# Optimization experiments

Hardware: AMD Instinct MI355X
Metric: run time of the kernel (lower is better)

The kernel has to match this reference:

```python
import jax, jax.numpy as jnp
import numpy as np

N_NODES = 20000
N_EDGES = 160000
N_GRAPHS = 64
IN_DIM = 128
HID = 512
N_ACT = 32


def gcn_conv(x, W, b, src, dst, n_nodes):
    # PyG GCNConv: add self-loops, symmetric normalization, x @ W then scatter-add.
    loop = jnp.arange(n_nodes, dtype=src.dtype)
    s = jnp.concatenate([src, loop])
    d = jnp.concatenate([dst, loop])
    deg = jax.ops.segment_sum(jnp.ones_like(d, dtype=x.dtype), d, num_segments=n_nodes)
    dinv = jnp.where(deg > 0, jax.lax.rsqrt(deg), 0.0)
    norm = dinv[s] * dinv[d]                      # [E+N]
    h = x @ W                                     # [N, out]
    msg = h[s] * norm[:, None]                    # gather + scale
    out = jax.ops.segment_sum(msg, d, num_segments=n_nodes)
    return out + b


def setup_inputs() -> dict:
    key = jax.random.key(0)
    ks = jax.random.split(key, 16)
    tree_x = jax.random.normal(ks[0], (N_NODES, IN_DIM), dtype=jnp.float32)
    edge_index = jax.random.randint(ks[1], (2, N_EDGES), 0, N_NODES, dtype=jnp.int32)
    # batch assignment: guarantee every graph id appears, then sort
    raw = jnp.concatenate([jnp.arange(N_GRAPHS, dtype=jnp.int32),
                           jax.random.randint(ks[2], (N_NODES - N_GRAPHS,), 0, N_GRAPHS, dtype=jnp.int32)])
    batch = jnp.sort(raw)

    def glorot(k, shape):
        lim = np.sqrt(6.0 / (shape[0] + shape[1]))
        return jax.random.uniform(k, shape, jnp.float32, -lim, lim)

    params = {
        'W1': glorot(ks[3], (IN_DIM, HID)), 'b1': jnp.zeros((HID,), jnp.float32),
        'W2': glorot(ks[4], (HID, HID)),    'b2': jnp.zeros((HID,), jnp.float32),
        'W3': glorot(ks[5], (HID, HID)),    'b3': jnp.zeros((HID,), jnp.float32),
        'Wf1': glorot(ks[6], (HID, HID)),   'bf1': jnp.zeros((HID,), jnp.float32),
        'Wf2': glorot(ks[7], (HID, HID)),   'bf2': jnp.zeros((HID,), jnp.float32),
        'Wf3': glorot(ks[8], (HID, HID)),   'bf3': jnp.zeros((HID,), jnp.float32),
        'Wo': glorot(ks[9], (HID, N_ACT)),  'bo': jnp.zeros((N_ACT,), jnp.float32),
    }
    return {'tree_x': tree_x, 'edge_index': edge_index, 'batch': batch, **params}


def reference(tree_x, edge_index, batch, W1, b1, W2, b2, W3, b3,
              Wf1, bf1, Wf2, bf2, Wf3, bf3, Wo, bo):
    src, dst = edge_index[0], edge_index[1]
    h = jax.nn.relu(gcn_conv(tree_x, W1, b1, src, dst, N_NODES))
    h = jax.nn.relu(gcn_conv(h, W2, b2, src, dst, N_NODES))
    h = jax.nn.relu(gcn_conv(h, W3, b3, src, dst, N_NODES))
    x = jax.ops.segment_max(h, batch, num_segments=N_GRAPHS)  # global_max_pool
    x = jax.nn.relu(x @ Wf1 + bf1)
    x = jax.nn.relu(x @ Wf2 + bf2)
    x = jax.nn.relu(x @ Wf3 + bf3)
    return x @ Wo + bo
```

## Files before the change

kernel.cpp:

```cpp
#include <hip/hip_runtime.h>
#include <stdint.h>

#define N_NODES 20000
#define N_EDGES 160000
#define N_GRAPHS 64
#define IN_DIM 128
#define HID 512
#define N_ACT 32

#define SCAN_NB ((N_NODES + 255) / 256)

typedef __attribute__((ext_vector_type(8))) short short8;
typedef __attribute__((ext_vector_type(4))) float f32x4;

__device__ __forceinline__ float bf2f(uint h16) {
    union { uint u; float f; } v; v.u = h16 << 16; return v.f;
}
__device__ __forceinline__ float bflo(uint u) {
    union { uint x; float f; } v; v.x = u << 16; return v.f;
}
__device__ __forceinline__ float bfhi(uint u) {
    union { uint x; float f; } v; v.x = u & 0xffff0000u; return v.f;
}
__device__ __forceinline__ ushort f2bf(float f) {
    union { float f; uint u; } v; v.f = f;
    uint u = v.u;
    uint r = (u + 0x7fffu + ((u >> 16) & 1u)) >> 16;
    return (ushort)r;
}

__device__ __forceinline__ void add8(float* acc, uint4 v) {
    acc[0] += bflo(v.x); acc[1] += bfhi(v.x);
    acc[2] += bflo(v.y); acc[3] += bfhi(v.y);
    acc[4] += bflo(v.z); acc[5] += bfhi(v.z);
    acc[6] += bflo(v.w); acc[7] += bfhi(v.w);
}


#define PB_HIST   625
#define PB_F2BF   (PB_HIST + 10000)
#define PB_WT1    (PB_F2BF + 256)
#define PB_WT2    (PB_WT1 + 1024)
#define PB_WT3    (PB_WT2 + 1024)
#define PB_BOUNDS (PB_WT3 + SCAN_NB)

__global__ __launch_bounds__(256) void k_prep(
    const int* __restrict__ edst, int* __restrict__ cnt,
    const float* __restrict__ tree_x, ushort* __restrict__ xbf,
    const float* __restrict__ W1, ushort* __restrict__ w1t,
    const float* __restrict__ W2, ushort* __restrict__ w2t,
    const float* __restrict__ W3, ushort* __restrict__ w3t,
    const int* __restrict__ batch, int* __restrict__ gstart)
{
    int b = blockIdx.x;
    int t = threadIdx.x;
    if (b < PB_HIST) {
        int e = b * 256 + t;
        if (e < N_EDGES) atomicAdd(&cnt[edst[e]], 1);
    } else if (b < PB_F2BF) {
        int i = (b - PB_HIST) * 256 + t;
        if (i < N_NODES * IN_DIM) xbf[i] = f2bf(tree_x[i]);
    } else if (b < PB_WT1) {
        int i = (b - PB_F2BF) * 256 + t;
        int n = i / IN_DIM, k = i % IN_DIM;
        w1t[i] = f2bf(W1[k * HID + n]);
    } else if (b < PB_WT2) {
        int i = (b - PB_WT1) * 256 + t;
        int n = i / HID, k = i % HID;
        w2t[i] = f2bf(W2[k * HID + n]);
    } else if (b < PB_WT3) {
        int i = (b - PB_WT2) * 256 + t;
        int n = i / HID, k = i % HID;
        w3t[i] = f2bf(W3[k * HID + n]);
    } else {
        int i = (b - PB_WT3) * 256 + t;
        if (i < N_NODES) {
            if (i == 0) {
                gstart[batch[0]] = 0;
                gstart[N_GRAPHS] = N_NODES;
            } else if (batch[i] != batch[i - 1]) {
                gstart[batch[i]] = i;
            }
        }
    }
}


__global__ __launch_bounds__(256) void k_part(const int* __restrict__ cnt, int* __restrict__ bsum) {
    __shared__ int s[256];
    int idx = blockIdx.x * 256 + threadIdx.x;
    s[threadIdx.x] = (idx < N_NODES) ? cnt[idx] : 0;
    __syncthreads();
    for (int off = 128; off > 0; off >>= 1) {
        if (threadIdx.x < off) s[threadIdx.x] += s[threadIdx.x + off];
        __syncthreads();
    }
    if (threadIdx.x == 0) bsum[blockIdx.x] = s[0];
}

__global__ __launch_bounds__(128) void k_scanb(const int* __restrict__ bsum,
                                               int* __restrict__ boff, int* __restrict__ rowstart) {
    __shared__ int s[128];
    int t = threadIdx.x;
    int own = (t < SCAN_NB) ? bsum[t] : 0;
    s[t] = own;
    __syncthreads();
    for (int off = 1; off < 128; off <<= 1) {
        int v = 0;
        if (t >= off) v = s[t - off];
        __syncthreads();
        s[t] += v;
        __syncthreads();
    }
    if (t < SCAN_NB) boff[t] = s[t] - own;
    if (t == SCAN_NB - 1) rowstart[N_NODES] = s[t];
}

__global__ __launch_bounds__(256) void k_final(
    const int* __restrict__ cnt, const int* __restrict__ boff,
    int* __restrict__ rowstart, int* __restrict__ cursor, float* __restrict__ dinv)
{
    __shared__ int s[256];
    int t = threadIdx.x;
    int idx = blockIdx.x * 256 + t;
    int c = (idx < N_NODES) ? cnt[idx] : 0;
    s[t] = c;
    __syncthreads();
    for (int off = 1; off < 256; off <<= 1) {
        int v = 0;
        if (t >= off) v = s[t - off];
        __syncthreads();
        s[t] += v;
        __syncthreads();
    }
    if (idx < N_NODES) {
        int start = boff[blockIdx.x] + s[t] - c;
        rowstart[idx] = start;
        cursor[idx] = start;
        dinv[idx] = rsqrtf((float)c + 1.0f);
    }
}

__global__ void k_fill(const int* __restrict__ src, const int* __restrict__ dst,
                       int* __restrict__ cursor, int* __restrict__ csr_src) {
    int e = blockIdx.x * 256 + threadIdx.x;
    if (e < N_EDGES) {
        int p = atomicAdd(&cursor[dst[e]], 1);
        csr_src[p] = src[e];
    }
}


__global__ __launch_bounds__(256) void k_gemm(
    const ushort* __restrict__ A, const ushort* __restrict__ Bt,
    const float* __restrict__ dinv, const float* __restrict__ bias,
    ushort* __restrict__ Out, int M, int Kdim, int mode)
{
    const int N = HID;
    __shared__ __align__(16) ushort lA[128 * 64];
    __shared__ __align__(16) ushort lB[128 * 64];
    int bm = blockIdx.x, bn = blockIdx.y;
    int tid = threadIdx.x;
    int wave = tid >> 6, lane = tid & 63;
    int wm = (wave >> 1) * 64, wn = (wave & 1) * 64;

    f32x4 acc[4][4] = {};

    int srow = lane >> 3;
    int scol = (lane & 7) * 8;

    for (int kt = 0; kt < Kdim; kt += 64) {
        for (int c = wave * 4; c < wave * 4 + 4; ++c) {
            int row = c * 8 + srow;
            int ga = bm * 128 + row; if (ga >= M) ga = M - 1;
            const ushort* gsA = A + (size_t)ga * Kdim + kt + scol;
            __builtin_amdgcn_global_load_lds(
                (const __attribute__((address_space(1))) void*)gsA,
                (__attribute__((address_space(3))) void*)(lA + c * 512), 16, 0, 0);
            int gb = bn * 128 + row;
            const ushort* gsB = Bt + (size_t)gb * Kdim + kt + scol;
            __builtin_amdgcn_global_load_lds(
                (const __attribute__((address_space(1))) void*)gsB,
                (__attribute__((address_space(3))) void*)(lB + c * 512), 16, 0, 0);
        }
        __syncthreads();
        for (int kk = 0; kk < 2; ++kk) {
            short8 af[4], bfr[4];
            int ko = kk * 32 + (lane >> 4) * 8;
            for (int m = 0; m < 4; ++m)
                af[m] = *(const short8*)&lA[(wm + m * 16 + (lane & 15)) * 64 + ko];
            for (int n = 0; n < 4; ++n)
                bfr[n] = *(const short8*)&lB[(wn + n * 16 + (lane & 15)) * 64 + ko];
            for (int m = 0; m < 4; ++m)
                for (int n = 0; n < 4; ++n)
                    acc[m][n] = __builtin_amdgcn_mfma_f32_16x16x32_bf16(af[m], bfr[n], acc[m][n], 0, 0, 0);
        }
        __syncthreads();
    }

    int cb = bn * 128 + wn + (lane & 15);
    float bb[4];
    if (mode == 1) {
        for (int n = 0; n < 4; ++n) bb[n] = bias[cb + n * 16];
    }
    for (int m = 0; m < 4; ++m) {
        int rbase = bm * 128 + wm + m * 16 + (lane >> 4) * 4;
        for (int j = 0; j < 4; ++j) {
            int r = rbase + j;
            if (r < M) {
                if (mode == 0) {
                    float dv = dinv[r];
                    for (int n = 0; n < 4; ++n)
                        Out[(size_t)r * N + cb + n * 16] = f2bf(acc[m][n][j] * dv);
                } else {
                    for (int n = 0; n < 4; ++n)
                        Out[(size_t)r * N + cb + n * 16] = f2bf(fmaxf(acc[m][n][j] + bb[n], 0.0f));
                }
            }
        }
    }
}


__global__ __launch_bounds__(256) void k_agg1(
    const ushort* __restrict__ Xin, const int* __restrict__ rowstart,
    const int* __restrict__ csr_src, const float* __restrict__ dinv,
    ushort* __restrict__ Y)
{
    int i = blockIdx.x * 4 + (threadIdx.x >> 6);
    if (i >= N_NODES) return;
    int lane = threadIdx.x & 63;
    const uint* xin = (const uint*)Xin;
    float dv = dinv[i];
    uint xi = xin[(size_t)i * 64 + lane];
    float a0 = dv * bflo(xi), a1 = dv * bfhi(xi);
    int e = rowstart[i], s1 = rowstart[i + 1];
    for (; e + 4 <= s1; e += 4) {
        int sa = csr_src[e], sb = csr_src[e + 1], sc = csr_src[e + 2], sd = csr_src[e + 3];
        float da = dinv[sa], db = dinv[sb], dc = dinv[sc], dd = dinv[sd];
        uint wa = xin[(size_t)sa * 64 + lane];
        uint wb = xin[(size_t)sb * 64 + lane];
        uint wc = xin[(size_t)sc * 64 + lane];
        uint wd = xin[(size_t)sd * 64 + lane];
        a0 = fmaf(da, bflo(wa), a0); a1 = fmaf(da, bfhi(wa), a1);
        a0 = fmaf(db, bflo(wb), a0); a1 = fmaf(db, bfhi(wb), a1);
        a0 = fmaf(dc, bflo(wc), a0); a1 = fmaf(dc, bfhi(wc), a1);
        a0 = fmaf(dd, bflo(wd), a0); a1 = fmaf(dd, bfhi(wd), a1);
    }
    for (; e < s1; ++e) {
        int sa = csr_src[e];
        float da = dinv[sa];
        uint wa = xin[(size_t)sa * 64 + lane];
        a0 = fmaf(da, bflo(wa), a0); a1 = fmaf(da, bfhi(wa), a1);
    }
    uint o = (uint)f2bf(dv * a0) | ((uint)f2bf(dv * a1) << 16);
    ((uint*)Y)[(size_t)i * 64 + lane] = o;
}


__global__ __launch_bounds__(256) void k_agg(
    const ushort* __restrict__ G, const int* __restrict__ rowstart,
    const int* __restrict__ csr_src, const float* __restrict__ dinv,
    const float* __restrict__ bias, ushort* __restrict__ X)
{
    int i = blockIdx.x * 4 + (threadIdx.x >> 6);
    if (i >= N_NODES) return;
    int lane = threadIdx.x & 63;
    const uint4* g4 = (const uint4*)G;

    uint4 a = g4[(size_t)i * 64 + lane];
    float acc[8] = { bflo(a.x), bfhi(a.x), bflo(a.y), bfhi(a.y),
                     bflo(a.z), bfhi(a.z), bflo(a.w), bfhi(a.w) };

    int e = rowstart[i], s1 = rowstart[i + 1];
    for (; e + 4 <= s1; e += 4) {
        int sa = csr_src[e], sb = csr_src[e + 1], sc = csr_src[e + 2], sd = csr_src[e + 3];
        uint4 wa = g4[(size_t)sa * 64 + lane];
        uint4 wb = g4[(size_t)sb * 64 + lane];
        uint4 wc = g4[(size_t)sc * 64 + lane];
        uint4 wd = g4[(size_t)sd * 64 + lane];
        add8(acc, wa); add8(acc, wb); add8(acc, wc); add8(acc, wd);
    }
    for (; e < s1; ++e) {
        int sa = csr_src[e];
        uint4 wa = g4[(size_t)sa * 64 + lane];
        add8(acc, wa);
    }

    float dv = dinv[i];
    float4 b0 = *(const float4*)(bias + lane * 8);
    float4 b1 = *(const float4*)(bias + lane * 8 + 4);
    float bb[8] = { b0.x, b0.y, b0.z, b0.w, b1.x, b1.y, b1.z, b1.w };

    uint4 o;
    uint p[8];
    for (int j = 0; j < 8; ++j)
        p[j] = f2bf(fmaxf(fmaf(dv, acc[j], bb[j]), 0.0f));
    o.x = p[0] | (p[1] << 16);
    o.y = p[2] | (p[3] << 16);
    o.z = p[4] | (p[5] << 16);
    o.w = p[6] | (p[7] << 16);
    *(uint4*)(X + (size_t)i * HID + lane * 8) = o;
}


__global__ __launch_bounds__(64) void k_pool(
    const ushort* __restrict__ X, const int* __restrict__ gstart, float* __restrict__ P)
{
    int g = blockIdx.x;
    int ch = blockIdx.y * 64 + threadIdx.x;
    float mx = -1e30f;
    int i0 = gstart[g], i1 = gstart[g + 1];
    int i = i0;
    for (; i + 4 <= i1; i += 4) {
        float a = bf2f(X[(size_t)(i + 0) * HID + ch]);
        float b = bf2f(X[(size_t)(i + 1) * HID + ch]);
        float c = bf2f(X[(size_t)(i + 2) * HID + ch]);
        float d = bf2f(X[(size_t)(i + 3) * HID + ch]);
        mx = fmaxf(mx, fmaxf(fmaxf(a, b), fmaxf(c, d)));
    }
    for (; i < i1; ++i) mx = fmaxf(mx, bf2f(X[(size_t)i * HID + ch]));
    P[(size_t)g * HID + ch] = mx;
}


__global__ __launch_bounds__(256) void k_fc(
    const float* __restrict__ in, const float* __restrict__ W,
    const float* __restrict__ b, float* __restrict__ out,
    int K, int NO, int relu)
{
    __shared__ float xs[HID];
    __shared__ float part[4][64];
    int g = blockIdx.x;
    int j0 = blockIdx.y * 64;
    int tid = threadIdx.x;
    int wave = tid >> 6, lane = tid & 63;

    for (int k = tid; k < K; k += 256) xs[k] = in[(size_t)g * K + k];
    __syncthreads();

    int j = j0 + lane;
    bool active = (j < NO);
    int kpw = K >> 2;
    int k0 = wave * kpw;
    float acc = 0.0f;
    if (active) {
        const float* wp = W + (size_t)k0 * NO + j;
        int k = 0;
        for (; k + 4 <= kpw; k += 4) {
            float w0 = wp[(size_t)(k + 0) * NO];
            float w1 = wp[(size_t)(k + 1) * NO];
            float w2 = wp[(size_t)(k + 2) * NO];
            float w3 = wp[(size_t)(k + 3) * NO];
            acc = fmaf(xs[k0 + k + 0], w0, acc);
            acc = fmaf(xs[k0 + k + 1], w1, acc);
            acc = fmaf(xs[k0 + k + 2], w2, acc);
            acc = fmaf(xs[k0 + k + 3], w3, acc);
        }
        for (; k < kpw; ++k)
            acc = fmaf(xs[k0 + k], wp[(size_t)k * NO], acc);
    }
    part[wave][lane] = acc;
    __syncthreads();
    if (wave == 0 && active) {
        float a = part[0][lane] + part[1][lane] + part[2][lane] + part[3][lane] + b[j];
        if (relu) a = fmaxf(a, 0.0f);
        out[(size_t)g * NO + j] = a;
    }
}


extern "C" void kernel_launch(void* const* d_in, const int* in_sizes, int n_in,
                              void* d_out, int out_size, void* d_ws, size_t ws_size,
                              hipStream_t stream) {
    const float* tree_x = (const float*)d_in[0];
    const int*   ei     = (const int*)d_in[1];
    const int*   batch  = (const int*)d_in[2];
    const float* W1  = (const float*)d_in[3];  const float* b1  = (const float*)d_in[4];
    const float* W2  = (const float*)d_in[5];  const float* b2  = (const float*)d_in[6];
    const float* W3  = (const float*)d_in[7];  const float* b3  = (const float*)d_in[8];
    const float* Wf1 = (const float*)d_in[9];  const float* bf1 = (const float*)d_in[10];
    const float* Wf2 = (const float*)d_in[11]; const float* bf2 = (const float*)d_in[12];
    const float* Wf3 = (const float*)d_in[13]; const float* bf3 = (const float*)d_in[14];
    const float* Wo  = (const float*)d_in[15]; const float* bo  = (const float*)d_in[16];

    char* w = (char*)d_ws;
    size_t off = 0;
    auto alloc = [&](size_t bytes) -> void* {
        void* p = w + off;
        off += (bytes + 255) & ~(size_t)255;
        return p;
    };
    int*    cnt      = (int*)alloc((size_t)N_NODES * 4);
    int*    cursor   = (int*)alloc((size_t)N_NODES * 4);
    int*    rowstart = (int*)alloc((size_t)(N_NODES + 1) * 4);
    float*  dinv     = (float*)alloc((size_t)N_NODES * 4);
    int*    csr      = (int*)alloc((size_t)N_EDGES * 4);
    int*    gstart   = (int*)alloc((size_t)(N_GRAPHS + 1) * 4);
    int*    bsum     = (int*)alloc((size_t)SCAN_NB * 4);
    int*    boff     = (int*)alloc((size_t)SCAN_NB * 4);
    ushort* xbf      = (ushort*)alloc((size_t)N_NODES * IN_DIM * 2);
    ushort* ybuf     = (ushort*)alloc((size_t)N_NODES * IN_DIM * 2);
    ushort* w1t      = (ushort*)alloc((size_t)HID * IN_DIM * 2);
    ushort* w2t      = (ushort*)alloc((size_t)HID * HID * 2);
    ushort* w3t      = (ushort*)alloc((size_t)HID * HID * 2);
    ushort* gbuf     = (ushort*)alloc((size_t)N_NODES * HID * 2);
    ushort* xbuf     = (ushort*)alloc((size_t)N_NODES * HID * 2);
    float*  P0       = (float*)alloc((size_t)N_GRAPHS * HID * 4);
    float*  P1       = (float*)alloc((size_t)N_GRAPHS * HID * 4);

    const int* esrc = ei;
    const int* edst = ei + N_EDGES;

    hipMemsetAsync(cnt, 0, (size_t)N_NODES * 4, stream);
    k_prep<<<PB_BOUNDS, 256, 0, stream>>>(edst, cnt, tree_x, xbf,
                                          W1, w1t, W2, w2t, W3, w3t, batch, gstart);
    k_part<<<SCAN_NB, 256, 0, stream>>>(cnt, bsum);
    k_scanb<<<1, 128, 0, stream>>>(bsum, boff, rowstart);
    k_final<<<SCAN_NB, 256, 0, stream>>>(cnt, boff, rowstart, cursor, dinv);
    k_fill<<<(N_EDGES + 255) / 256, 256, 0, stream>>>(esrc, edst, cursor, csr);

    dim3 gemm_grid((N_NODES + 127) / 128, HID / 128);

    k_agg1<<<N_NODES / 4, 256, 0, stream>>>(xbf, rowstart, csr, dinv, ybuf);
    k_gemm<<<gemm_grid, 256, 0, stream>>>(ybuf, w1t, dinv, b1, xbuf, N_NODES, IN_DIM, 1);
    k_gemm<<<gemm_grid, 256, 0, stream>>>(xbuf, w2t, dinv, b2, gbuf, N_NODES, HID, 0);
    k_agg<<<N_NODES / 4, 256, 0, stream>>>(gbuf, rowstart, csr, dinv, b2, xbuf);
    k_gemm<<<gemm_grid, 256, 0, stream>>>(xbuf, w3t, dinv, b3, gbuf, N_NODES, HID, 0);
    k_agg<<<N_NODES / 4, 256, 0, stream>>>(gbuf, rowstart, csr, dinv, b3, xbuf);

    k_pool<<<dim3(N_GRAPHS, 8), 64, 0, stream>>>(xbuf, gstart, P0);

    k_fc<<<dim3(N_GRAPHS, HID / 64), 256, 0, stream>>>(P0, Wf1, bf1, P1, HID, HID, 1);
    k_fc<<<dim3(N_GRAPHS, HID / 64), 256, 0, stream>>>(P1, Wf2, bf2, P0, HID, HID, 1);
    k_fc<<<dim3(N_GRAPHS, HID / 64), 256, 0, stream>>>(P0, Wf3, bf3, P1, HID, HID, 1);
    k_fc<<<dim3(N_GRAPHS, 1), 256, 0, stream>>>(P1, Wo, bo, (float*)d_out, HID, N_ACT, 0);
}
```

Before: 239.4 us.

## Fuse pooling and MLP head into one kernel, tile weight transposes, unroll gather

Replaces the pool kernel and four FC launches with a single per-graph kernel that max-pools into shared memory and runs the three hidden layers plus the output layer in place. This removes four launches and the round trips through global intermediates. The trade-off is only 64 blocks, with each block streaming all weight matrices serially. The weight transposes in the prep kernel now go through 32x32 shared-memory tiles so both reads and writes are coalesced, and the aggregation gather loop is unrolled by 8 for more memory-level parallelism. The pooled max now starts at 0 instead of a large negative value, which is valid only because the inputs are post-ReLU.

```diff
diff --git a/kernel.cpp b/kernel.cpp
--- a/kernel.cpp
+++ b/kernel.cpp
@@ -39,9 +39,9 @@
 
 #define PB_HIST   625
 #define PB_F2BF   (PB_HIST + 10000)
-#define PB_WT1    (PB_F2BF + 256)
-#define PB_WT2    (PB_WT1 + 1024)
-#define PB_WT3    (PB_WT2 + 1024)
+#define PB_WT1    (PB_F2BF + 64)
+#define PB_WT2    (PB_WT1 + 256)
+#define PB_WT3    (PB_WT2 + 256)
 #define PB_BOUNDS (PB_WT3 + SCAN_NB)
 
 __global__ __launch_bounds__(256) void k_prep(
@@ -52,8 +52,10 @@
     const float* __restrict__ W3, ushort* __restrict__ w3t,
     const int* __restrict__ batch, int* __restrict__ gstart)
 {
+    __shared__ float lds[32][33];
     int b = blockIdx.x;
     int t = threadIdx.x;
+    int r = t >> 5, c = t & 31;
     if (b < PB_HIST) {
         int e = b * 256 + t;
         if (e < N_EDGES) atomicAdd(&cnt[edst[e]], 1);
@@ -61,17 +63,29 @@
         int i = (b - PB_HIST) * 256 + t;
         if (i < N_NODES * IN_DIM) xbf[i] = f2bf(tree_x[i]);
     } else if (b < PB_WT1) {
-        int i = (b - PB_F2BF) * 256 + t;
-        int n = i / IN_DIM, k = i % IN_DIM;
-        w1t[i] = f2bf(W1[k * HID + n]);
+        int tt = b - PB_F2BF;
+        int kt = tt & 3, nt = tt >> 2;
+        for (int rr = r; rr < 32; rr += 8)
+            lds[rr][c] = W1[(size_t)(kt * 32 + rr) * HID + nt * 32 + c];
+        __syncthreads();
+        for (int rr = r; rr < 32; rr += 8)
+            w1t[(size_t)(nt * 32 + rr) * IN_DIM + kt * 32 + c] = f2bf(lds[c][rr]);
     } else if (b < PB_WT2) {
-        int i = (b - PB_WT1) * 256 + t;
-        int n = i / HID, k = i % HID;
-        w2t[i] = f2bf(W2[k * HID + n]);
+        int tt = b - PB_WT1;
+        int kt = tt & 15, nt = tt >> 4;
+        for (int rr = r; rr < 32; rr += 8)
+            lds[rr][c] = W2[(size_t)(kt * 32 + rr) * HID + nt * 32 + c];
+        __syncthreads();
+        for (int rr = r; rr < 32; rr += 8)
+            w2t[(size_t)(nt * 32 + rr) * HID + kt * 32 + c] = f2bf(lds[c][rr]);
     } else if (b < PB_WT3) {
-        int i = (b - PB_WT2) * 256 + t;
-        int n = i / HID, k = i % HID;
-        w3t[i] = f2bf(W3[k * HID + n]);
+        int tt = b - PB_WT2;
+        int kt = tt & 15, nt = tt >> 4;
+        for (int rr = r; rr < 32; rr += 8)
+            lds[rr][c] = W3[(size_t)(kt * 32 + rr) * HID + nt * 32 + c];
+        __syncthreads();
+        for (int rr = r; rr < 32; rr += 8)
+            w3t[(size_t)(nt * 32 + rr) * HID + kt * 32 + c] = f2bf(lds[c][rr]);
     } else {
         int i = (b - PB_WT3) * 256 + t;
         if (i < N_NODES) {
@@ -273,18 +287,32 @@
                      bflo(a.z), bfhi(a.z), bflo(a.w), bfhi(a.w) };
 
     int e = rowstart[i], s1 = rowstart[i + 1];
+    for (; e + 8 <= s1; e += 8) {
+        int s0 = csr_src[e],     s1i = csr_src[e + 1], s2 = csr_src[e + 2], s3 = csr_src[e + 3];
+        int s4 = csr_src[e + 4], s5 = csr_src[e + 5],  s6 = csr_src[e + 6], s7 = csr_src[e + 7];
+        uint4 w0 = g4[(size_t)s0 * 64 + lane];
+        uint4 w1 = g4[(size_t)s1i * 64 + lane];
+        uint4 w2 = g4[(size_t)s2 * 64 + lane];
+        uint4 w3 = g4[(size_t)s3 * 64 + lane];
+        uint4 w4 = g4[(size_t)s4 * 64 + lane];
+        uint4 w5 = g4[(size_t)s5 * 64 + lane];
+        uint4 w6 = g4[(size_t)s6 * 64 + lane];
+        uint4 w7 = g4[(size_t)s7 * 64 + lane];
+        add8(acc, w0); add8(acc, w1); add8(acc, w2); add8(acc, w3);
+        add8(acc, w4); add8(acc, w5); add8(acc, w6); add8(acc, w7);
+    }
     for (; e + 4 <= s1; e += 4) {
-        int sa = csr_src[e], sb = csr_src[e + 1], sc = csr_src[e + 2], sd = csr_src[e + 3];
-        uint4 wa = g4[(size_t)sa * 64 + lane];
-        uint4 wb = g4[(size_t)sb * 64 + lane];
-        uint4 wc = g4[(size_t)sc * 64 + lane];
-        uint4 wd = g4[(size_t)sd * 64 + lane];
-        add8(acc, wa); add8(acc, wb); add8(acc, wc); add8(acc, wd);
+        int s0 = csr_src[e], s1i = csr_src[e + 1], s2 = csr_src[e + 2], s3 = csr_src[e + 3];
+        uint4 w0 = g4[(size_t)s0 * 64 + lane];
+        uint4 w1 = g4[(size_t)s1i * 64 + lane];
+        uint4 w2 = g4[(size_t)s2 * 64 + lane];
+        uint4 w3 = g4[(size_t)s3 * 64 + lane];
+        add8(acc, w0); add8(acc, w1); add8(acc, w2); add8(acc, w3);
     }
     for (; e < s1; ++e) {
-        int sa = csr_src[e];
-        uint4 wa = g4[(size_t)sa * 64 + lane];
-        add8(acc, wa);
+        int s0 = csr_src[e];
+        uint4 w0 = g4[(size_t)s0 * 64 + lane];
+        add8(acc, w0);
     }
 
     float dv = dinv[i];
@@ -304,68 +332,59 @@
 }
 
 
-__global__ __launch_bounds__(64) void k_pool(
-    const ushort* __restrict__ X, const int* __restrict__ gstart, float* __restrict__ P)
-{
-    int g = blockIdx.x;
-    int ch = blockIdx.y * 64 + threadIdx.x;
-    float mx = -1e30f;
+__global__ __launch_bounds__(256) void k_head(
+    const ushort* __restrict__ X, const int* __restrict__ gstart,
+    const float* __restrict__ Wf1, const float* __restrict__ bf1,
+    const float* __restrict__ Wf2, const float* __restrict__ bf2,
+    const float* __restrict__ Wf3, const float* __restrict__ bf3,
+    const float* __restrict__ Wo, const float* __restrict__ bo,
+    float* __restrict__ out)
+{
+    __shared__ float xs[HID];
+    __shared__ float ys[HID];
+    __shared__ float red[256];
+    int g = blockIdx.x, t = threadIdx.x;
+
     int i0 = gstart[g], i1 = gstart[g + 1];
-    int i = i0;
-    for (; i + 4 <= i1; i += 4) {
-        float a = bf2f(X[(size_t)(i + 0) * HID + ch]);
-        float b = bf2f(X[(size_t)(i + 1) * HID + ch]);
-        float c = bf2f(X[(size_t)(i + 2) * HID + ch]);
-        float d = bf2f(X[(size_t)(i + 3) * HID + ch]);
-        mx = fmaxf(mx, fmaxf(fmaxf(a, b), fmaxf(c, d)));
-    }
-    for (; i < i1; ++i) mx = fmaxf(mx, bf2f(X[(size_t)i * HID + ch]));
-    P[(size_t)g * HID + ch] = mx;
-}
-
-
-__global__ __launch_bounds__(256) void k_fc(
-    const float* __restrict__ in, const float* __restrict__ W,
-    const float* __restrict__ b, float* __restrict__ out,
-    int K, int NO, int relu)
-{
-    __shared__ float xs[HID];
-    __shared__ float part[4][64];
-    int g = blockIdx.x;
-    int j0 = blockIdx.y * 64;
-    int tid = threadIdx.x;
-    int wave = tid >> 6, lane = tid & 63;
-
-    for (int k = tid; k < K; k += 256) xs[k] = in[(size_t)g * K + k];
+    float m0 = 0.0f, m1 = 0.0f;
+    for (int i = i0; i < i1; ++i) {
+        const ushort* row = X + (size_t)i * HID;
+        m0 = fmaxf(m0, bf2f(row[t]));
+        m1 = fmaxf(m1, bf2f(row[t + 256]));
+    }
+    xs[t] = m0; xs[t + 256] = m1;
     __syncthreads();
 
-    int j = j0 + lane;
-    bool active = (j < NO);
-    int kpw = K >> 2;
-    int k0 = wave * kpw;
-    float acc = 0.0f;
-    if (active) {
-        const float* wp = W + (size_t)k0 * NO + j;
-        int k = 0;
-        for (; k + 4 <= kpw; k += 4) {
-            float w0 = wp[(size_t)(k + 0) * NO];
-            float w1 = wp[(size_t)(k + 1) * NO];
-            float w2 = wp[(size_t)(k + 2) * NO];
-            float w3 = wp[(size_t)(k + 3) * NO];
-            acc = fmaf(xs[k0 + k + 0], w0, acc);
-            acc = fmaf(xs[k0 + k + 1], w1, acc);
-            acc = fmaf(xs[k0 + k + 2], w2, acc);
-            acc = fmaf(xs[k0 + k + 3], w3, acc);
+    auto fc = [&](const float* __restrict__ Wm, const float* __restrict__ bv,
+                  const float* in, float* outv) {
+        float a0 = bv[t], a1 = bv[t + 256];
+        float c0 = 0.0f, c1 = 0.0f;
+        for (int k = 0; k < HID; k += 2) {
+            float x0 = in[k], x1 = in[k + 1];
+            const float* w0 = Wm + (size_t)k * HID;
+            a0 = fmaf(x0, w0[t], a0);
+            a1 = fmaf(x0, w0[t + 256], a1);
+            c0 = fmaf(x1, w0[HID + t], c0);
+            c1 = fmaf(x1, w0[HID + t + 256], c1);
         }
-        for (; k < kpw; ++k)
-            acc = fmaf(xs[k0 + k], wp[(size_t)k * NO], acc);
-    }
-    part[wave][lane] = acc;
+        outv[t] = fmaxf(a0 + c0, 0.0f);
+        outv[t + 256] = fmaxf(a1 + c1, 0.0f);
+        __syncthreads();
+    };
+    fc(Wf1, bf1, xs, ys);
+    fc(Wf2, bf2, ys, xs);
+    fc(Wf3, bf3, xs, ys);
+
+    int j = t & 31, kg = t >> 5;
+    float a = 0.0f;
+    for (int k = kg * 64; k < kg * 64 + 64; ++k)
+        a = fmaf(ys[k], Wo[(size_t)k * N_ACT + j], a);
+    red[t] = a;
     __syncthreads();
-    if (wave == 0 && active) {
-        float a = part[0][lane] + part[1][lane] + part[2][lane] + part[3][lane] + b[j];
-        if (relu) a = fmaxf(a, 0.0f);
-        out[(size_t)g * NO + j] = a;
+    if (t < 32) {
+        float s = bo[t];
+        for (int q = 0; q < 8; ++q) s += red[q * 32 + t];
+        out[(size_t)g * N_ACT + t] = s;
     }
 }
 
@@ -406,8 +425,6 @@
     ushort* w3t      = (ushort*)alloc((size_t)HID * HID * 2);
     ushort* gbuf     = (ushort*)alloc((size_t)N_NODES * HID * 2);
     ushort* xbuf     = (ushort*)alloc((size_t)N_NODES * HID * 2);
-    float*  P0       = (float*)alloc((size_t)N_GRAPHS * HID * 4);
-    float*  P1       = (float*)alloc((size_t)N_GRAPHS * HID * 4);
 
     const int* esrc = ei;
     const int* edst = ei + N_EDGES;
@@ -429,10 +446,6 @@
     k_gemm<<<gemm_grid, 256, 0, stream>>>(xbuf, w3t, dinv, b3, gbuf, N_NODES, HID, 0);
     k_agg<<<N_NODES / 4, 256, 0, stream>>>(gbuf, rowstart, csr, dinv, b3, xbuf);
 
-    k_pool<<<dim3(N_GRAPHS, 8), 64, 0, stream>>>(xbuf, gstart, P0);
-
-    k_fc<<<dim3(N_GRAPHS, HID / 64), 256, 0, stream>>>(P0, Wf1, bf1, P1, HID, HID, 1);
-    k_fc<<<dim3(N_GRAPHS, HID / 64), 256, 0, stream>>>(P1, Wf2, bf2, P0, HID, HID, 1);
-    k_fc<<<dim3(N_GRAPHS, HID / 64), 256, 0, stream>>>(P0, Wf3, bf3, P1, HID, HID, 1);
-    k_fc<<<dim3(N_GRAPHS, 1), 256, 0, stream>>>(P1, Wo, bo, (float*)d_out, HID, N_ACT, 0);
-}
+    k_head<<<N_GRAPHS, 256, 0, stream>>>(xbuf, gstart, Wf1, bf1, Wf2, bf2,
+                                         Wf3, bf3, Wo, bo, (float*)d_out);
+}
```

Result: slower. 326.2 us (+36.2%).
